# Optimization experiments

Hardware: AMD Instinct MI355X
Metric: run time of the kernel (lower is better)

## Reference

```python
import jax, jax.numpy as jnp
import numpy as np

N = 1024
D = 128          # node_dim
NUM_LAYERS = 3
H_CLS = 128      # edge classifier hidden


def setup_inputs() -> dict:
    key = jax.random.key(0)
    ks = jax.random.split(key, 20)
    s_in = 1.0 / np.sqrt(3.0)
    s_d = 1.0 / np.sqrt(D)
    s_2d = 1.0 / np.sqrt(2 * D)
    s_h = 1.0 / np.sqrt(H_CLS)
    inp = {
        "node_features": jax.random.uniform(ks[0], (N, 3), jnp.float32),
        "adj_matrix": jax.random.uniform(ks[1], (N, N), jnp.float32),
        "edge_weights": jax.random.normal(ks[2], (N, N, 1), jnp.float32),
        # node embedding Linear(3, D)
        "W_embed": jax.random.uniform(ks[3], (3, D), jnp.float32, -s_in, s_in),
        "b_embed": jax.random.uniform(ks[4], (D,), jnp.float32, -s_in, s_in),
        # stacked GCN layer params, [L, ...]
        "Wu": jax.random.uniform(ks[5], (NUM_LAYERS, D, D), jnp.float32, -s_d, s_d),
        "bu": jax.random.uniform(ks[6], (NUM_LAYERS, D), jnp.float32, -s_d, s_d),
        "Wv": jax.random.uniform(ks[7], (NUM_LAYERS, D, D), jnp.float32, -s_d, s_d),
        "bv": jax.random.uniform(ks[8], (NUM_LAYERS, D), jnp.float32, -s_d, s_d),
        "Wg": jax.random.uniform(ks[9], (NUM_LAYERS, 2 * D, D), jnp.float32, -s_2d, s_2d),
        "bg": jax.random.uniform(ks[10], (NUM_LAYERS, D), jnp.float32, -s_2d, s_2d),
        # edge classifier: Linear(2D, 128) -> ReLU -> Linear(128, 1)
        "Wc1": jax.random.uniform(ks[11], (2 * D, H_CLS), jnp.float32, -s_2d, s_2d),
        "bc1": jax.random.uniform(ks[12], (H_CLS,), jnp.float32, -s_2d, s_2d),
        "Wc2": jax.random.uniform(ks[13], (H_CLS, 1), jnp.float32, -s_h, s_h),
        "bc2": jax.random.uniform(ks[14], (1,), jnp.float32, -s_h, s_h),
    }
    return inp


def reference(node_features, adj_matrix, edge_weights,
              W_embed, b_embed, Wu, bu, Wv, bv, Wg, bg,
              Wc1, bc1, Wc2, bc2):
    h = node_features @ W_embed + b_embed                       # [N, D]
    for l in range(NUM_LAYERS):
        u = h @ Wu[l] + bu[l]                                   # [N, D]
        v = h @ Wv[l] + bv[l]                                   # [N, D]
        agg = adj_matrix @ v                                    # [N, D]
        # gate Linear(2D, D) on cat([u, agg]) == u @ Wg[:D] + agg @ Wg[D:]
        gate = jax.nn.sigmoid(u @ Wg[l, :D] + agg @ Wg[l, D:] + bg[l])
        h = jax.nn.relu(h + gate * agg)
    # edge classifier: cat([h_i, h_j]) @ Wc1 == (h @ Wc1[:D])[i] + (h @ Wc1[D:])[j]
    hi = h @ Wc1[:D]                                            # [N, H]
    hj = h @ Wc1[D:]                                            # [N, H]
    hidden = jax.nn.relu(hi[:, None, :] + hj[None, :, :] + bc1) # [N, N, H]
    logits = jnp.einsum('ijh,h->ij', hidden, Wc2[:, 0]) + bc2[0]  # [N, N]
    loss = jnp.mean(jnp.square(logits * adj_matrix - edge_weights[..., 0]))
    return logits, loss
```

## Files before the change

kernel.cpp:

```cpp
#include <hip/hip_runtime.h>

#define NN 1024
#define DD 128

typedef __attribute__((ext_vector_type(8))) __bf16 bf16x8;
typedef __attribute__((ext_vector_type(4))) float f32x4;

__device__ __forceinline__ float us2f(unsigned short b) { return __uint_as_float(((unsigned)b) << 16); }
__device__ __forceinline__ unsigned short f2bf(float f) {
    unsigned x = __float_as_uint(f);
    return (unsigned short)((x + 0x7fffu + ((x >> 16) & 1u)) >> 16);
}

__global__ __launch_bounds__(256) void k_prep_embuv(
    const float* __restrict__ adj, unsigned short* __restrict__ aH, unsigned short* __restrict__ aL,
    const float* __restrict__ nf, const float* __restrict__ We, const float* __restrict__ be,
    const float* __restrict__ Wu, const float* __restrict__ bu,
    const float* __restrict__ Wv, const float* __restrict__ bv,
    float* __restrict__ h, float* __restrict__ u,
    unsigned short* __restrict__ vTh, unsigned short* __restrict__ vTl,
    float* __restrict__ lossAcc, unsigned* __restrict__ counter)
{
    __shared__ float hS[4][DD];
    int b = blockIdx.x, tid = threadIdx.x;
    if (b < 1024) {
        int idx = (b * 256 + tid) * 4;
        float4 a = *(const float4*)(adj + idx);
        ushort4 hv, lv;
        hv.x = f2bf(a.x); lv.x = f2bf(a.x - us2f(hv.x));
        hv.y = f2bf(a.y); lv.y = f2bf(a.y - us2f(hv.y));
        hv.z = f2bf(a.z); lv.z = f2bf(a.z - us2f(hv.z));
        hv.w = f2bf(a.w); lv.w = f2bf(a.w - us2f(hv.w));
        *(ushort4*)(aH + idx) = hv;
        *(ushort4*)(aL + idx) = lv;
        if (b == 0 && tid == 0) { *lossAcc = 0.f; *counter = 0u; }
        return;
    }
    int m0 = (b - 1024) * 4;
    int d = tid & 127, half = tid >> 7;
    float hr[4];
#pragma unroll
    for (int r = 0; r < 4; ++r) {
        float a = be[d];
#pragma unroll
        for (int k = 0; k < 3; ++k) a = fmaf(nf[(m0 + r) * 3 + k], We[k * DD + d], a);
        hr[r] = a;
    }
    if (half == 0) {
#pragma unroll
        for (int r = 0; r < 4; ++r) { h[(m0 + r) * DD + d] = hr[r]; hS[r][d] = hr[r]; }
    }
    __syncthreads();
    const float* W = half ? Wv : Wu;
    float acc[4] = {0.f, 0.f, 0.f, 0.f};
#pragma unroll 4
    for (int k4 = 0; k4 < DD; k4 += 4) {
        f32x4 h0 = *(const f32x4*)&hS[0][k4];
        f32x4 h1 = *(const f32x4*)&hS[1][k4];
        f32x4 h2 = *(const f32x4*)&hS[2][k4];
        f32x4 h3 = *(const f32x4*)&hS[3][k4];
#pragma unroll
        for (int kk = 0; kk < 4; ++kk) {
            float w = W[(k4 + kk) * DD + d];
            acc[0] = fmaf(h0[kk], w, acc[0]);
            acc[1] = fmaf(h1[kk], w, acc[1]);
            acc[2] = fmaf(h2[kk], w, acc[2]);
            acc[3] = fmaf(h3[kk], w, acc[3]);
        }
    }
    if (half == 0) {
        float bb = bu[d];
#pragma unroll
        for (int r = 0; r < 4; ++r) u[(m0 + r) * DD + d] = acc[r] + bb;
    } else {
        float bb = bv[d];
        float v0 = acc[0] + bb, v1 = acc[1] + bb, v2 = acc[2] + bb, v3 = acc[3] + bb;
        ushort4 hv, lv;
        hv.x = f2bf(v0); lv.x = f2bf(v0 - us2f(hv.x));
        hv.y = f2bf(v1); lv.y = f2bf(v1 - us2f(hv.y));
        hv.z = f2bf(v2); lv.z = f2bf(v2 - us2f(hv.z));
        hv.w = f2bf(v3); lv.w = f2bf(v3 - us2f(hv.w));
        *(ushort4*)(vTh + d * NN + m0) = hv;
        *(ushort4*)(vTl + d * NN + m0) = lv;
    }
}

__global__ __launch_bounds__(256) void k_agg(
    const unsigned short* __restrict__ adjH, const unsigned short* __restrict__ adjL,
    const unsigned short* __restrict__ vTh, const unsigned short* __restrict__ vTl,
    float* __restrict__ P)
{
    int tid = threadIdx.x, lane = tid & 63, w = tid >> 6;
    int b = blockIdx.x;
    int nt = b >> 7;
    int mt = (b >> 1) & 63;
    int kc = ((b & 1) << 2) | w;
    int m = lane & 15, quad = lane >> 4;
    int k0 = kc * 128 + quad * 8;
    const unsigned short* ah = adjH + (size_t)(mt * 16 + m) * NN + k0;
    const unsigned short* al = adjL + (size_t)(mt * 16 + m) * NN + k0;
    const unsigned short* bh = vTh + (size_t)(nt * 16 + m) * NN + k0;
    const unsigned short* bl = vTl + (size_t)(nt * 16 + m) * NN + k0;
    f32x4 acc = {0.f, 0.f, 0.f, 0.f};
#pragma unroll
    for (int kt = 0; kt < 4; ++kt) {
        bf16x8 aH = *(const bf16x8*)(ah + kt * 32);
        bf16x8 aL = *(const bf16x8*)(al + kt * 32);
        bf16x8 bH = *(const bf16x8*)(bh + kt * 32);
        bf16x8 bL = *(const bf16x8*)(bl + kt * 32);
        acc = __builtin_amdgcn_mfma_f32_16x16x32_bf16(aH, bH, acc, 0, 0, 0);
        acc = __builtin_amdgcn_mfma_f32_16x16x32_bf16(aH, bL, acc, 0, 0, 0);
        acc = __builtin_amdgcn_mfma_f32_16x16x32_bf16(aL, bH, acc, 0, 0, 0);
    }
    float* Pk = P + (size_t)kc * (NN * DD);
    int row0 = mt * 16 + quad * 4;
    int col = nt * 16 + m;
#pragma unroll
    for (int r = 0; r < 4; ++r) Pk[(row0 + r) * DD + col] = acc[r];
}

__global__ __launch_bounds__(256) void k_gateuv(
    const float* __restrict__ P, float* __restrict__ u, float* __restrict__ h,
    const float* __restrict__ Wg, const float* __restrict__ bg,
    const float* __restrict__ Wun, const float* __restrict__ bun,
    const float* __restrict__ Wvn, const float* __restrict__ bvn,
    unsigned short* __restrict__ vTh, unsigned short* __restrict__ vTl)
{
    __shared__ float uS[4][DD], aS[4][DD], hS[4][DD];
    int tid = threadIdx.x;
    int m0 = blockIdx.x * 4;
    int d = tid & 127, half = tid >> 7;
#pragma unroll
    for (int e = tid; e < 512; e += 256) {
        int r = e >> 7, dd = e & 127;
        int idx = (m0 + r) * DD + dd;
        float s = 0.f;
#pragma unroll
        for (int c = 0; c < 8; ++c) s += P[(size_t)c * (NN * DD) + idx];
        aS[r][dd] = s;
        uS[r][dd] = u[idx];
    }
    __syncthreads();
    const float* WA = Wg;
    const float* WB = Wg + DD * DD;
    int r0 = half * 2;
    float acc[2] = {0.f, 0.f};
#pragma unroll 4
    for (int k4 = 0; k4 < DD; k4 += 4) {
        f32x4 u0 = *(const f32x4*)&uS[r0][k4];
        f32x4 u1 = *(const f32x4*)&uS[r0 + 1][k4];
        f32x4 a0 = *(const f32x4*)&aS[r0][k4];
        f32x4 a1 = *(const f32x4*)&aS[r0 + 1][k4];
#pragma unroll
        for (int kk = 0; kk < 4; ++kk) {
            float wa = WA[(k4 + kk) * DD + d];
            float wb = WB[(k4 + kk) * DD + d];
            acc[0] = fmaf(u0[kk], wa, fmaf(a0[kk], wb, acc[0]));
            acc[1] = fmaf(u1[kk], wa, fmaf(a1[kk], wb, acc[1]));
        }
    }
    float bgd = bg[d];
#pragma unroll
    for (int rr = 0; rr < 2; ++rr) {
        int r = r0 + rr;
        float g = 1.f / (1.f + __expf(-(acc[rr] + bgd)));
        float nh = fmaf(g, aS[r][d], h[(m0 + r) * DD + d]);
        nh = nh > 0.f ? nh : 0.f;
        h[(m0 + r) * DD + d] = nh;
        hS[r][d] = nh;
    }
    __syncthreads();
    const float* W = half ? Wvn : Wun;
    float av[4] = {0.f, 0.f, 0.f, 0.f};
#pragma unroll 4
    for (int k4 = 0; k4 < DD; k4 += 4) {
        f32x4 h0 = *(const f32x4*)&hS[0][k4];
        f32x4 h1 = *(const f32x4*)&hS[1][k4];
        f32x4 h2 = *(const f32x4*)&hS[2][k4];
        f32x4 h3 = *(const f32x4*)&hS[3][k4];
#pragma unroll
        for (int kk = 0; kk < 4; ++kk) {
            float w = W[(k4 + kk) * DD + d];
            av[0] = fmaf(h0[kk], w, av[0]);
            av[1] = fmaf(h1[kk], w, av[1]);
            av[2] = fmaf(h2[kk], w, av[2]);
            av[3] = fmaf(h3[kk], w, av[3]);
        }
    }
    if (half == 0) {
        float bb = bun[d];
#pragma unroll
        for (int r = 0; r < 4; ++r) u[(m0 + r) * DD + d] = av[r] + bb;
    } else {
        float bb = bvn[d];
        float v0 = av[0] + bb, v1 = av[1] + bb, v2 = av[2] + bb, v3 = av[3] + bb;
        ushort4 hv, lv;
        hv.x = f2bf(v0); lv.x = f2bf(v0 - us2f(hv.x));
        hv.y = f2bf(v1); lv.y = f2bf(v1 - us2f(hv.y));
        hv.z = f2bf(v2); lv.z = f2bf(v2 - us2f(hv.z));
        hv.w = f2bf(v3); lv.w = f2bf(v3 - us2f(hv.w));
        *(ushort4*)(vTh + d * NN + m0) = hv;
        *(ushort4*)(vTl + d * NN + m0) = lv;
    }
}

__global__ __launch_bounds__(256) void k_gatecls(
    const float* __restrict__ P, float* __restrict__ u, float* __restrict__ h,
    const float* __restrict__ Wg, const float* __restrict__ bg,
    const float* __restrict__ Wc1, const float* __restrict__ bc1, const float* __restrict__ Wc2,
    float* __restrict__ hi, float* __restrict__ hj,
    float* __restrict__ S1, float* __restrict__ S2)
{
    __shared__ float uS[4][DD], aS[4][DD], hS[4][DD];
    __shared__ float sred[2][4];
    int tid = threadIdx.x;
    int m0 = blockIdx.x * 4;
    int d = tid & 127, half = tid >> 7;
    if (tid < 8) sred[tid >> 2][tid & 3] = 0.f;
#pragma unroll
    for (int e = tid; e < 512; e += 256) {
        int r = e >> 7, dd = e & 127;
        int idx = (m0 + r) * DD + dd;
        float s = 0.f;
#pragma unroll
        for (int c = 0; c < 8; ++c) s += P[(size_t)c * (NN * DD) + idx];
        aS[r][dd] = s;
        uS[r][dd] = u[idx];
    }
    __syncthreads();
    const float* WA = Wg;
    const float* WB = Wg + DD * DD;
    int r0 = half * 2;
    float acc[2] = {0.f, 0.f};
#pragma unroll 4
    for (int k4 = 0; k4 < DD; k4 += 4) {
        f32x4 u0 = *(const f32x4*)&uS[r0][k4];
        f32x4 u1 = *(const f32x4*)&uS[r0 + 1][k4];
        f32x4 a0 = *(const f32x4*)&aS[r0][k4];
        f32x4 a1 = *(const f32x4*)&aS[r0 + 1][k4];
#pragma unroll
        for (int kk = 0; kk < 4; ++kk) {
            float wa = WA[(k4 + kk) * DD + d];
            float wb = WB[(k4 + kk) * DD + d];
            acc[0] = fmaf(u0[kk], wa, fmaf(a0[kk], wb, acc[0]));
            acc[1] = fmaf(u1[kk], wa, fmaf(a1[kk], wb, acc[1]));
        }
    }
    float bgd = bg[d];
#pragma unroll
    for (int rr = 0; rr < 2; ++rr) {
        int r = r0 + rr;
        float g = 1.f / (1.f + __expf(-(acc[rr] + bgd)));
        float nh = fmaf(g, aS[r][d], h[(m0 + r) * DD + d]);
        nh = nh > 0.f ? nh : 0.f;
        hS[r][d] = nh;
    }
    __syncthreads();
    const float* W = Wc1 + (half ? DD * DD : 0);
    float av[4] = {0.f, 0.f, 0.f, 0.f};
#pragma unroll 4
    for (int k4 = 0; k4 < DD; k4 += 4) {
        f32x4 h0 = *(const f32x4*)&hS[0][k4];
        f32x4 h1 = *(const f32x4*)&hS[1][k4];
        f32x4 h2 = *(const f32x4*)&hS[2][k4];
        f32x4 h3 = *(const f32x4*)&hS[3][k4];
#pragma unroll
        for (int kk = 0; kk < 4; ++kk) {
            float w = W[(k4 + kk) * DD + d];
            av[0] = fmaf(h0[kk], w, av[0]);
            av[1] = fmaf(h1[kk], w, av[1]);
            av[2] = fmaf(h2[kk], w, av[2]);
            av[3] = fmaf(h3[kk], w, av[3]);
        }
    }
    float wv = Wc2[d];
    float bcv = half ? 0.f : bc1[d];
    float* out = half ? hj : hi;
    int lane = tid & 63;
#pragma unroll
    for (int r = 0; r < 4; ++r) {
        float val = av[r] + bcv;
        out[(m0 + r) * DD + d] = val;
        float p = val * wv;
#pragma unroll
        for (int off = 32; off; off >>= 1) p += __shfl_down(p, off);
        if (lane == 0) atomicAdd(&sred[half][r], p);
    }
    __syncthreads();
    if (tid < 4) S1[m0 + tid] = sred[0][tid];
    else if (tid < 8) S2[m0 + tid - 4] = sred[1][tid - 4];
}

__global__ __launch_bounds__(256) void k_edge(
    const float* __restrict__ hi, const float* __restrict__ hj,
    const float* __restrict__ S1, const float* __restrict__ S2,
    const float* __restrict__ Wc2, const float* __restrict__ bc2,
    const float* __restrict__ adj, const float* __restrict__ ew,
    float* __restrict__ outL, float* __restrict__ lossAcc, unsigned* __restrict__ counter)
{
    __shared__ float hiT[128][68];
    __shared__ float hjT[128][68];
    __shared__ float wS[128];
    __shared__ float lred;
    int tid = threadIdx.x;
    int i0 = (blockIdx.x >> 4) * 64, j0 = (blockIdx.x & 15) * 64;
    if (tid == 0) lred = 0.f;
    if (tid < 128) wS[tid] = Wc2[tid];
    for (int e = tid; e < 64 * 128; e += 256) {
        int r = e >> 7, hh = e & 127;
        hiT[hh][r] = hi[(i0 + r) * DD + hh];
        hjT[hh][r] = hj[(j0 + r) * DD + hh];
    }
    __syncthreads();
    int tx = tid & 15, ty = tid >> 4;
    float acc[4][4] = {};
#pragma unroll 4
    for (int hh = 0; hh < 128; ++hh) {
        f32x4 a = *(const f32x4*)&hiT[hh][ty * 4];
        f32x4 b = *(const f32x4*)&hjT[hh][tx * 4];
        float w = wS[hh];
#pragma unroll
        for (int p = 0; p < 4; ++p)
#pragma unroll
            for (int q = 0; q < 4; ++q) {
                float x = a[p] + b[q];
                acc[p][q] = fmaf(fabsf(x), w, acc[p][q]);
            }
    }
    float bcv = bc2[0];
    float ls = 0.f;
#pragma unroll
    for (int p = 0; p < 4; ++p) {
        int i = i0 + ty * 4 + p;
        float s1 = S1[i];
        int jb = j0 + tx * 4;
        f32x4 s2 = *(const f32x4*)(S2 + jb);
        f32x4 lg;
#pragma unroll
        for (int q = 0; q < 4; ++q)
            lg[q] = fmaf(0.5f, acc[p][q] + s1 + s2[q], bcv);
        *(f32x4*)(outL + (size_t)i * NN + jb) = lg;
        f32x4 a4 = *(const f32x4*)(adj + (size_t)i * NN + jb);
        f32x4 e4 = *(const f32x4*)(ew + (size_t)i * NN + jb);
#pragma unroll
        for (int q = 0; q < 4; ++q) {
            float t = fmaf(lg[q], a4[q], -e4[q]);
            ls = fmaf(t, t, ls);
        }
    }
#pragma unroll
    for (int off = 32; off; off >>= 1) ls += __shfl_down(ls, off);
    if ((tid & 63) == 0) atomicAdd(&lred, ls);
    __syncthreads();
    if (tid == 0) {
        atomicAdd(lossAcc, lred);
        __threadfence();
        unsigned old = atomicAdd(counter, 1u);
        if (old == 255u) {
            __threadfence();
            outL[(size_t)NN * NN] = (*(volatile float*)lossAcc) * (1.f / (1024.f * 1024.f));
        }
    }
}

extern "C" void kernel_launch(void* const* d_in, const int* in_sizes, int n_in,
                              void* d_out, int out_size, void* d_ws, size_t ws_size,
                              hipStream_t stream)
{
    const float* nf  = (const float*)d_in[0];
    const float* adj = (const float*)d_in[1];
    const float* ew  = (const float*)d_in[2];
    const float* We  = (const float*)d_in[3];
    const float* be  = (const float*)d_in[4];
    const float* Wu  = (const float*)d_in[5];
    const float* bu  = (const float*)d_in[6];
    const float* Wv  = (const float*)d_in[7];
    const float* bv  = (const float*)d_in[8];
    const float* Wg  = (const float*)d_in[9];
    const float* bg  = (const float*)d_in[10];
    const float* Wc1 = (const float*)d_in[11];
    const float* bc1 = (const float*)d_in[12];
    const float* Wc2 = (const float*)d_in[13];
    const float* bc2 = (const float*)d_in[14];

    float* ws = (float*)d_ws;
    float* h   = ws;
    float* u   = ws + 131072;
    unsigned short* vTh = (unsigned short*)(ws + 262144);
    unsigned short* vTl = (unsigned short*)(ws + 327680);
    float* P   = ws + 393216;
    unsigned short* adjH = (unsigned short*)(ws + 1441792);
    unsigned short* adjL = (unsigned short*)(ws + 1966080);
    float* hi  = ws + 2490368;
    float* hj  = ws + 2621440;
    float* S1  = ws + 2752512;
    float* S2  = ws + 2753536;
    float* lossAcc = ws + 2754560;
    unsigned* counter = (unsigned*)(ws + 2754561);

    k_prep_embuv<<<1280, 256, 0, stream>>>(adj, adjH, adjL, nf, We, be,
                                           Wu, bu, Wv, bv, h, u, vTh, vTl, lossAcc, counter);
    for (int l = 0; l < 3; ++l) {
        k_agg<<<1024, 256, 0, stream>>>(adjH, adjL, vTh, vTl, P);
        if (l < 2)
            k_gateuv<<<256, 256, 0, stream>>>(P, u, h, Wg + l * 32768, bg + l * 128,
                                              Wu + (l + 1) * 16384, bu + (l + 1) * 128,
                                              Wv + (l + 1) * 16384, bv + (l + 1) * 128,
                                              vTh, vTl);
        else
            k_gatecls<<<256, 256, 0, stream>>>(P, u, h, Wg + 2 * 32768, bg + 2 * 128,
                                               Wc1, bc1, Wc2, hi, hj, S1, S2);
    }
    k_edge<<<256, 256, 0, stream>>>(hi, hj, S1, S2, Wc2, bc2, adj, ew,
                                    (float*)d_out, lossAcc, counter);
}
```

Baseline: 187.2 us.

## Fuse all stages into one persistent kernel with software grid barriers

Replaces the eight separate launches (prep, three agg plus gate kernels, edge) with a single 256-block persistent kernel that separates stages with atomic-counter grid barriers, after a memset of the control words. Per-layer buffers are triple-buffered so later stages never overwrite data that other blocks are still reading. The aggregation split changes from eight K-chunks written to a global partial buffer to two K-chunks reduced in shared memory, which removes the 8-way partial-sum traffic. The risks are lower parallelism in the aggregation stage (256 blocks instead of 1024), spin-wait barrier cost, and a deadlock hazard if the 256 blocks are not all resident at once.

Measured after the change: 344.2 us. 83.9% more time.

```diff
diff --git a/kernel.cpp b/kernel.cpp
--- a/kernel.cpp
+++ b/kernel.cpp
@@ -12,353 +12,320 @@
     return (unsigned short)((x + 0x7fffu + ((x >> 16) & 1u)) >> 16);
 }
 
-__global__ __launch_bounds__(256) void k_prep_embuv(
-    const float* __restrict__ adj, unsigned short* __restrict__ aH, unsigned short* __restrict__ aL,
-    const float* __restrict__ nf, const float* __restrict__ We, const float* __restrict__ be,
-    const float* __restrict__ Wu, const float* __restrict__ bu,
-    const float* __restrict__ Wv, const float* __restrict__ bv,
-    float* __restrict__ h, float* __restrict__ u,
-    unsigned short* __restrict__ vTh, unsigned short* __restrict__ vTl,
-    float* __restrict__ lossAcc, unsigned* __restrict__ counter)
-{
-    __shared__ float hS[4][DD];
-    int b = blockIdx.x, tid = threadIdx.x;
-    if (b < 1024) {
-        int idx = (b * 256 + tid) * 4;
-        float4 a = *(const float4*)(adj + idx);
-        ushort4 hv, lv;
-        hv.x = f2bf(a.x); lv.x = f2bf(a.x - us2f(hv.x));
-        hv.y = f2bf(a.y); lv.y = f2bf(a.y - us2f(hv.y));
-        hv.z = f2bf(a.z); lv.z = f2bf(a.z - us2f(hv.z));
-        hv.w = f2bf(a.w); lv.w = f2bf(a.w - us2f(hv.w));
-        *(ushort4*)(aH + idx) = hv;
-        *(ushort4*)(aL + idx) = lv;
-        if (b == 0 && tid == 0) { *lossAcc = 0.f; *counter = 0u; }
-        return;
-    }
-    int m0 = (b - 1024) * 4;
-    int d = tid & 127, half = tid >> 7;
-    float hr[4];
-#pragma unroll
-    for (int r = 0; r < 4; ++r) {
-        float a = be[d];
-#pragma unroll
-        for (int k = 0; k < 3; ++k) a = fmaf(nf[(m0 + r) * 3 + k], We[k * DD + d], a);
-        hr[r] = a;
-    }
-    if (half == 0) {
-#pragma unroll
-        for (int r = 0; r < 4; ++r) { h[(m0 + r) * DD + d] = hr[r]; hS[r][d] = hr[r]; }
+struct SEdge { float hiT[128][68]; float hjT[128][68]; float wS[128]; float lred; };
+struct SGate { float uS[4][DD]; float aS[4][DD]; float hS[4][DD]; float sred[2][4]; };
+struct SAgg  { float red[4][64][4]; };
+union SU { SEdge edge; SGate gate; SAgg agg; float hS[4][DD]; };
+
+__device__ __forceinline__ void gridbar(unsigned* bar, unsigned target, int tid) {
+    __syncthreads();
+    if (tid == 0) {
+        __threadfence();
+        __hip_atomic_fetch_add(bar, 1u, __ATOMIC_RELEASE, __HIP_MEMORY_SCOPE_AGENT);
+        while (__hip_atomic_load(bar, __ATOMIC_ACQUIRE, __HIP_MEMORY_SCOPE_AGENT) < target)
+            __builtin_amdgcn_s_sleep(1);
+        __threadfence();
     }
     __syncthreads();
-    const float* W = half ? Wv : Wu;
-    float acc[4] = {0.f, 0.f, 0.f, 0.f};
-#pragma unroll 4
-    for (int k4 = 0; k4 < DD; k4 += 4) {
-        f32x4 h0 = *(const f32x4*)&hS[0][k4];
-        f32x4 h1 = *(const f32x4*)&hS[1][k4];
-        f32x4 h2 = *(const f32x4*)&hS[2][k4];
-        f32x4 h3 = *(const f32x4*)&hS[3][k4];
-#pragma unroll
-        for (int kk = 0; kk < 4; ++kk) {
-            float w = W[(k4 + kk) * DD + d];
-            acc[0] = fmaf(h0[kk], w, acc[0]);
-            acc[1] = fmaf(h1[kk], w, acc[1]);
-            acc[2] = fmaf(h2[kk], w, acc[2]);
-            acc[3] = fmaf(h3[kk], w, acc[3]);
+}
+
+__global__ __launch_bounds__(256) void k_all(
+    const float* __restrict__ nf, const float* __restrict__ adj, const float* __restrict__ ew,
+    const float* __restrict__ We, const float* __restrict__ be,
+    const float* __restrict__ Wu_all, const float* __restrict__ bu_all,
+    const float* __restrict__ Wv_all, const float* __restrict__ bv_all,
+    const float* __restrict__ Wg_all, const float* __restrict__ bg_all,
+    const float* __restrict__ Wc1, const float* __restrict__ bc1,
+    const float* __restrict__ Wc2, const float* __restrict__ bc2,
+    float* __restrict__ hbuf, float* __restrict__ ubuf, float* __restrict__ aggbuf,
+    unsigned short* __restrict__ vthbuf, unsigned short* __restrict__ vtlbuf,
+    unsigned short* __restrict__ adjH, unsigned short* __restrict__ adjL,
+    float* __restrict__ hi, float* __restrict__ hj,
+    float* __restrict__ S1, float* __restrict__ S2,
+    unsigned* __restrict__ ctrl,
+    float* __restrict__ outL)
+{
+    __shared__ SU sh;
+    const int b = blockIdx.x, tid = threadIdx.x;
+    unsigned* bar = ctrl;
+    unsigned* edgeCnt = ctrl + 1;
+    float* lossAcc = (float*)(ctrl + 2);
+    const int d = tid & 127, half = tid >> 7;
+
+    {
+#pragma unroll
+        for (int i = 0; i < 4; ++i) {
+            int idx = b * 4096 + i * 1024 + tid * 4;
+            float4 a = *(const float4*)(adj + idx);
+            ushort4 hv, lv;
+            hv.x = f2bf(a.x); lv.x = f2bf(a.x - us2f(hv.x));
+            hv.y = f2bf(a.y); lv.y = f2bf(a.y - us2f(hv.y));
+            hv.z = f2bf(a.z); lv.z = f2bf(a.z - us2f(hv.z));
+            hv.w = f2bf(a.w); lv.w = f2bf(a.w - us2f(hv.w));
+            *(ushort4*)(adjH + idx) = hv;
+            *(ushort4*)(adjL + idx) = lv;
+        }
+        int m0 = b * 4;
+        if (half == 0) {
+#pragma unroll
+            for (int r = 0; r < 4; ++r) {
+                float a = be[d];
+#pragma unroll
+                for (int k = 0; k < 3; ++k) a = fmaf(nf[(m0 + r) * 3 + k], We[k * DD + d], a);
+                hbuf[(m0 + r) * DD + d] = a;
+                sh.hS[r][d] = a;
+            }
+        }
+        __syncthreads();
+        const float* W = half ? Wv_all : Wu_all;
+        float acc[4] = {0.f, 0.f, 0.f, 0.f};
+#pragma unroll 4
+        for (int k4 = 0; k4 < DD; k4 += 4) {
+            f32x4 h0 = *(const f32x4*)&sh.hS[0][k4];
+            f32x4 h1 = *(const f32x4*)&sh.hS[1][k4];
+            f32x4 h2 = *(const f32x4*)&sh.hS[2][k4];
+            f32x4 h3 = *(const f32x4*)&sh.hS[3][k4];
+#pragma unroll
+            for (int kk = 0; kk < 4; ++kk) {
+                float w = W[(k4 + kk) * DD + d];
+                acc[0] = fmaf(h0[kk], w, acc[0]);
+                acc[1] = fmaf(h1[kk], w, acc[1]);
+                acc[2] = fmaf(h2[kk], w, acc[2]);
+                acc[3] = fmaf(h3[kk], w, acc[3]);
+            }
+        }
+        if (half == 0) {
+            float bb = bu_all[d];
+#pragma unroll
+            for (int r = 0; r < 4; ++r) ubuf[(m0 + r) * DD + d] = acc[r] + bb;
+        } else {
+            float bb = bv_all[d];
+            float v0 = acc[0] + bb, v1 = acc[1] + bb, v2 = acc[2] + bb, v3 = acc[3] + bb;
+            ushort4 hv, lv;
+            hv.x = f2bf(v0); lv.x = f2bf(v0 - us2f(hv.x));
+            hv.y = f2bf(v1); lv.y = f2bf(v1 - us2f(hv.y));
+            hv.z = f2bf(v2); lv.z = f2bf(v2 - us2f(hv.z));
+            hv.w = f2bf(v3); lv.w = f2bf(v3 - us2f(hv.w));
+            *(ushort4*)(vthbuf + d * NN + m0) = hv;
+            *(ushort4*)(vtlbuf + d * NN + m0) = lv;
         }
     }
-    if (half == 0) {
-        float bb = bu[d];
-#pragma unroll
-        for (int r = 0; r < 4; ++r) u[(m0 + r) * DD + d] = acc[r] + bb;
-    } else {
-        float bb = bv[d];
-        float v0 = acc[0] + bb, v1 = acc[1] + bb, v2 = acc[2] + bb, v3 = acc[3] + bb;
-        ushort4 hv, lv;
-        hv.x = f2bf(v0); lv.x = f2bf(v0 - us2f(hv.x));
-        hv.y = f2bf(v1); lv.y = f2bf(v1 - us2f(hv.y));
-        hv.z = f2bf(v2); lv.z = f2bf(v2 - us2f(hv.z));
-        hv.w = f2bf(v3); lv.w = f2bf(v3 - us2f(hv.w));
-        *(ushort4*)(vTh + d * NN + m0) = hv;
-        *(ushort4*)(vTl + d * NN + m0) = lv;
+    unsigned tgt = 256;
+    gridbar(bar, tgt, tid); tgt += 256;
+
+    for (int l = 0; l < 3; ++l) {
+        const unsigned short* vth = vthbuf + l * (NN * DD);
+        const unsigned short* vtl = vtlbuf + l * (NN * DD);
+        float* aggl = aggbuf + l * (NN * DD);
+        const float* ul = ubuf + l * (NN * DD);
+        const float* hprev = hbuf + l * (NN * DD);
+
+        {
+            int w = tid >> 6, lane = tid & 63;
+            int mt = b & 63, np = b >> 6;
+            int nt = np * 2 + (w >> 1);
+            int kc = w & 1;
+            int m = lane & 15, quad = lane >> 4;
+            int k0 = kc * 512 + quad * 8;
+            const unsigned short* ah = adjH + (size_t)(mt * 16 + m) * NN + k0;
+            const unsigned short* al = adjL + (size_t)(mt * 16 + m) * NN + k0;
+            const unsigned short* bh = vth + (size_t)(nt * 16 + m) * NN + k0;
+            const unsigned short* bl = vtl + (size_t)(nt * 16 + m) * NN + k0;
+            f32x4 acc = {0.f, 0.f, 0.f, 0.f};
+#pragma unroll 4
+            for (int kt = 0; kt < 16; ++kt) {
+                bf16x8 aH = *(const bf16x8*)(ah + kt * 32);
+                bf16x8 aL = *(const bf16x8*)(al + kt * 32);
+                bf16x8 bH = *(const bf16x8*)(bh + kt * 32);
+                bf16x8 bL = *(const bf16x8*)(bl + kt * 32);
+                acc = __builtin_amdgcn_mfma_f32_16x16x32_bf16(aH, bH, acc, 0, 0, 0);
+                acc = __builtin_amdgcn_mfma_f32_16x16x32_bf16(aH, bL, acc, 0, 0, 0);
+                acc = __builtin_amdgcn_mfma_f32_16x16x32_bf16(aL, bH, acc, 0, 0, 0);
+            }
+            *(f32x4*)&sh.agg.red[w][lane][0] = acc;
+            __syncthreads();
+            if ((w & 1) == 0) {
+                f32x4 s = *(const f32x4*)&sh.agg.red[w][lane][0];
+                f32x4 t = *(const f32x4*)&sh.agg.red[w + 1][lane][0];
+                int row0 = mt * 16 + quad * 4;
+                int col = nt * 16 + m;
+#pragma unroll
+                for (int r = 0; r < 4; ++r) aggl[(row0 + r) * DD + col] = s[r] + t[r];
+            }
+        }
+        gridbar(bar, tgt, tid); tgt += 256;
+
+        {
+            int m0 = b * 4;
+            if (tid < 8) sh.gate.sred[tid >> 2][tid & 3] = 0.f;
+#pragma unroll
+            for (int e = tid; e < 512; e += 256) {
+                int r = e >> 7, dd = e & 127;
+                int idx = (m0 + r) * DD + dd;
+                sh.gate.aS[r][dd] = aggl[idx];
+                sh.gate.uS[r][dd] = ul[idx];
+            }
+            __syncthreads();
+            const float* WA = Wg_all + l * (2 * DD * DD);
+            const float* WB = WA + DD * DD;
+            int r0 = half * 2;
+            float acc[2] = {0.f, 0.f};
+#pragma unroll 4
+            for (int k4 = 0; k4 < DD; k4 += 4) {
+                f32x4 u0 = *(const f32x4*)&sh.gate.uS[r0][k4];
+                f32x4 u1 = *(const f32x4*)&sh.gate.uS[r0 + 1][k4];
+                f32x4 a0 = *(const f32x4*)&sh.gate.aS[r0][k4];
+                f32x4 a1 = *(const f32x4*)&sh.gate.aS[r0 + 1][k4];
+#pragma unroll
+                for (int kk = 0; kk < 4; ++kk) {
+                    float wa = WA[(k4 + kk) * DD + d];
+                    float wb = WB[(k4 + kk) * DD + d];
+                    acc[0] = fmaf(u0[kk], wa, fmaf(a0[kk], wb, acc[0]));
+                    acc[1] = fmaf(u1[kk], wa, fmaf(a1[kk], wb, acc[1]));
+                }
+            }
+            float bgd = bg_all[l * DD + d];
+#pragma unroll
+            for (int rr = 0; rr < 2; ++rr) {
+                int r = r0 + rr;
+                float g = 1.f / (1.f + __expf(-(acc[rr] + bgd)));
+                float nh = fmaf(g, sh.gate.aS[r][d], hprev[(m0 + r) * DD + d]);
+                nh = nh > 0.f ? nh : 0.f;
+                sh.gate.hS[r][d] = nh;
+                if (l < 2) hbuf[(l + 1) * (NN * DD) + (m0 + r) * DD + d] = nh;
+            }
+            __syncthreads();
+            if (l < 2) {
+                const float* W = half ? (Wv_all + (l + 1) * (DD * DD)) : (Wu_all + (l + 1) * (DD * DD));
+                float av[4] = {0.f, 0.f, 0.f, 0.f};
+#pragma unroll 4
+                for (int k4 = 0; k4 < DD; k4 += 4) {
+                    f32x4 h0 = *(const f32x4*)&sh.gate.hS[0][k4];
+                    f32x4 h1 = *(const f32x4*)&sh.gate.hS[1][k4];
+                    f32x4 h2 = *(const f32x4*)&sh.gate.hS[2][k4];
+                    f32x4 h3 = *(const f32x4*)&sh.gate.hS[3][k4];
+#pragma unroll
+                    for (int kk = 0; kk < 4; ++kk) {
+                        float w = W[(k4 + kk) * DD + d];
+                        av[0] = fmaf(h0[kk], w, av[0]);
+                        av[1] = fmaf(h1[kk], w, av[1]);
+                        av[2] = fmaf(h2[kk], w, av[2]);
+                        av[3] = fmaf(h3[kk], w, av[3]);
+                    }
+                }
+                if (half == 0) {
+                    float bb = bu_all[(l + 1) * DD + d];
+#pragma unroll
+                    for (int r = 0; r < 4; ++r)
+                        ubuf[(l + 1) * (NN * DD) + (m0 + r) * DD + d] = av[r] + bb;
+                } else {
+                    float bb = bv_all[(l + 1) * DD + d];
+                    float v0 = av[0] + bb, v1 = av[1] + bb, v2 = av[2] + bb, v3 = av[3] + bb;
+                    ushort4 hv, lv;
+                    hv.x = f2bf(v0); lv.x = f2bf(v0 - us2f(hv.x));
+                    hv.y = f2bf(v1); lv.y = f2bf(v1 - us2f(hv.y));
+                    hv.z = f2bf(v2); lv.z = f2bf(v2 - us2f(hv.z));
+                    hv.w = f2bf(v3); lv.w = f2bf(v3 - us2f(hv.w));
+                    *(ushort4*)(vthbuf + (l + 1) * (NN * DD) + d * NN + m0) = hv;
+                    *(ushort4*)(vtlbuf + (l + 1) * (NN * DD) + d * NN + m0) = lv;
+                }
+            } else {
+                const float* W = Wc1 + (half ? DD * DD : 0);
+                float av[4] = {0.f, 0.f, 0.f, 0.f};
+#pragma unroll 4
+                for (int k4 = 0; k4 < DD; k4 += 4) {
+                    f32x4 h0 = *(const f32x4*)&sh.gate.hS[0][k4];
+                    f32x4 h1 = *(const f32x4*)&sh.gate.hS[1][k4];
+                    f32x4 h2 = *(const f32x4*)&sh.gate.hS[2][k4];
+                    f32x4 h3 = *(const f32x4*)&sh.gate.hS[3][k4];
+#pragma unroll
+                    for (int kk = 0; kk < 4; ++kk) {
+                        float w = W[(k4 + kk) * DD + d];
+                        av[0] = fmaf(h0[kk], w, av[0]);
+                        av[1] = fmaf(h1[kk], w, av[1]);
+                        av[2] = fmaf(h2[kk], w, av[2]);
+                        av[3] = fmaf(h3[kk], w, av[3]);
+                    }
+                }
+                float wv = Wc2[d];
+                float bcv = half ? 0.f : bc1[d];
+                float* out = half ? hj : hi;
+                int lane = tid & 63;
+#pragma unroll
+                for (int r = 0; r < 4; ++r) {
+                    float val = av[r] + bcv;
+                    out[(m0 + r) * DD + d] = val;
+                    float p = val * wv;
+#pragma unroll
+                    for (int off = 32; off; off >>= 1) p += __shfl_down(p, off);
+                    if (lane == 0) atomicAdd(&sh.gate.sred[half][r], p);
+                }
+                __syncthreads();
+                if (tid < 4) S1[m0 + tid] = sh.gate.sred[0][tid];
+                else if (tid < 8) S2[m0 + tid - 4] = sh.gate.sred[1][tid - 4];
+            }
+        }
+        gridbar(bar, tgt, tid); tgt += 256;
     }
-}
-
-__global__ __launch_bounds__(256) void k_agg(
-    const unsigned short* __restrict__ adjH, const unsigned short* __restrict__ adjL,
-    const unsigned short* __restrict__ vTh, const unsigned short* __restrict__ vTl,
-    float* __restrict__ P)
-{
-    int tid = threadIdx.x, lane = tid & 63, w = tid >> 6;
-    int b = blockIdx.x;
-    int nt = b >> 7;
-    int mt = (b >> 1) & 63;
-    int kc = ((b & 1) << 2) | w;
-    int m = lane & 15, quad = lane >> 4;
-    int k0 = kc * 128 + quad * 8;
-    const unsigned short* ah = adjH + (size_t)(mt * 16 + m) * NN + k0;
-    const unsigned short* al = adjL + (size_t)(mt * 16 + m) * NN + k0;
-    const unsigned short* bh = vTh + (size_t)(nt * 16 + m) * NN + k0;
-    const unsigned short* bl = vTl + (size_t)(nt * 16 + m) * NN + k0;
-    f32x4 acc = {0.f, 0.f, 0.f, 0.f};
-#pragma unroll
-    for (int kt = 0; kt < 4; ++kt) {
-        bf16x8 aH = *(const bf16x8*)(ah + kt * 32);
-        bf16x8 aL = *(const bf16x8*)(al + kt * 32);
-        bf16x8 bH = *(const bf16x8*)(bh + kt * 32);
-        bf16x8 bL = *(const bf16x8*)(bl + kt * 32);
-        acc = __builtin_amdgcn_mfma_f32_16x16x32_bf16(aH, bH, acc, 0, 0, 0);
-        acc = __builtin_amdgcn_mfma_f32_16x16x32_bf16(aH, bL, acc, 0, 0, 0);
-        acc = __builtin_amdgcn_mfma_f32_16x16x32_bf16(aL, bH, acc, 0, 0, 0);
-    }
-    float* Pk = P + (size_t)kc * (NN * DD);
-    int row0 = mt * 16 + quad * 4;
-    int col = nt * 16 + m;
-#pragma unroll
-    for (int r = 0; r < 4; ++r) Pk[(row0 + r) * DD + col] = acc[r];
-}
-
-__global__ __launch_bounds__(256) void k_gateuv(
-    const float* __restrict__ P, float* __restrict__ u, float* __restrict__ h,
-    const float* __restrict__ Wg, const float* __restrict__ bg,
-    const float* __restrict__ Wun, const float* __restrict__ bun,
-    const float* __restrict__ Wvn, const float* __restrict__ bvn,
-    unsigned short* __restrict__ vTh, unsigned short* __restrict__ vTl)
-{
-    __shared__ float uS[4][DD], aS[4][DD], hS[4][DD];
-    int tid = threadIdx.x;
-    int m0 = blockIdx.x * 4;
-    int d = tid & 127, half = tid >> 7;
-#pragma unroll
-    for (int e = tid; e < 512; e += 256) {
-        int r = e >> 7, dd = e & 127;
-        int idx = (m0 + r) * DD + dd;
-        float s = 0.f;
-#pragma unroll
-        for (int c = 0; c < 8; ++c) s += P[(size_t)c * (NN * DD) + idx];
-        aS[r][dd] = s;
-        uS[r][dd] = u[idx];
-    }
-    __syncthreads();
-    const float* WA = Wg;
-    const float* WB = Wg + DD * DD;
-    int r0 = half * 2;
-    float acc[2] = {0.f, 0.f};
-#pragma unroll 4
-    for (int k4 = 0; k4 < DD; k4 += 4) {
-        f32x4 u0 = *(const f32x4*)&uS[r0][k4];
-        f32x4 u1 = *(const f32x4*)&uS[r0 + 1][k4];
-        f32x4 a0 = *(const f32x4*)&aS[r0][k4];
-        f32x4 a1 = *(const f32x4*)&aS[r0 + 1][k4];
-#pragma unroll
-        for (int kk = 0; kk < 4; ++kk) {
-            float wa = WA[(k4 + kk) * DD + d];
-            float wb = WB[(k4 + kk) * DD + d];
-            acc[0] = fmaf(u0[kk], wa, fmaf(a0[kk], wb, acc[0]));
-            acc[1] = fmaf(u1[kk], wa, fmaf(a1[kk], wb, acc[1]));
-        }
-    }
-    float bgd = bg[d];
-#pragma unroll
-    for (int rr = 0; rr < 2; ++rr) {
-        int r = r0 + rr;
-        float g = 1.f / (1.f + __expf(-(acc[rr] + bgd)));
-        float nh = fmaf(g, aS[r][d], h[(m0 + r) * DD + d]);
-        nh = nh > 0.f ? nh : 0.f;
-        h[(m0 + r) * DD + d] = nh;
-        hS[r][d] = nh;
-    }
-    __syncthreads();
-    const float* W = half ? Wvn : Wun;
-    float av[4] = {0.f, 0.f, 0.f, 0.f};
-#pragma unroll 4
-    for (int k4 = 0; k4 < DD; k4 += 4) {
-        f32x4 h0 = *(const f32x4*)&hS[0][k4];
-        f32x4 h1 = *(const f32x4*)&hS[1][k4];
-        f32x4 h2 = *(const f32x4*)&hS[2][k4];
-        f32x4 h3 = *(const f32x4*)&hS[3][k4];
-#pragma unroll
-        for (int kk = 0; kk < 4; ++kk) {
-            float w = W[(k4 + kk) * DD + d];
-            av[0] = fmaf(h0[kk], w, av[0]);
-            av[1] = fmaf(h1[kk], w, av[1]);
-            av[2] = fmaf(h2[kk], w, av[2]);
-            av[3] = fmaf(h3[kk], w, av[3]);
-        }
-    }
-    if (half == 0) {
-        float bb = bun[d];
-#pragma unroll
-        for (int r = 0; r < 4; ++r) u[(m0 + r) * DD + d] = av[r] + bb;
-    } else {
-        float bb = bvn[d];
-        float v0 = av[0] + bb, v1 = av[1] + bb, v2 = av[2] + bb, v3 = av[3] + bb;
-        ushort4 hv, lv;
-        hv.x = f2bf(v0); lv.x = f2bf(v0 - us2f(hv.x));
-        hv.y = f2bf(v1); lv.y = f2bf(v1 - us2f(hv.y));
-        hv.z = f2bf(v2); lv.z = f2bf(v2 - us2f(hv.z));
-        hv.w = f2bf(v3); lv.w = f2bf(v3 - us2f(hv.w));
-        *(ushort4*)(vTh + d * NN + m0) = hv;
-        *(ushort4*)(vTl + d * NN + m0) = lv;
-    }
-}
-
-__global__ __launch_bounds__(256) void k_gatecls(
-    const float* __restrict__ P, float* __restrict__ u, float* __restrict__ h,
-    const float* __restrict__ Wg, const float* __restrict__ bg,
-    const float* __restrict__ Wc1, const float* __restrict__ bc1, const float* __restrict__ Wc2,
-    float* __restrict__ hi, float* __restrict__ hj,
-    float* __restrict__ S1, float* __restrict__ S2)
-{
-    __shared__ float uS[4][DD], aS[4][DD], hS[4][DD];
-    __shared__ float sred[2][4];
-    int tid = threadIdx.x;
-    int m0 = blockIdx.x * 4;
-    int d = tid & 127, half = tid >> 7;
-    if (tid < 8) sred[tid >> 2][tid & 3] = 0.f;
-#pragma unroll
-    for (int e = tid; e < 512; e += 256) {
-        int r = e >> 7, dd = e & 127;
-        int idx = (m0 + r) * DD + dd;
-        float s = 0.f;
-#pragma unroll
-        for (int c = 0; c < 8; ++c) s += P[(size_t)c * (NN * DD) + idx];
-        aS[r][dd] = s;
-        uS[r][dd] = u[idx];
-    }
-    __syncthreads();
-    const float* WA = Wg;
-    const float* WB = Wg + DD * DD;
-    int r0 = half * 2;
-    float acc[2] = {0.f, 0.f};
-#pragma unroll 4
-    for (int k4 = 0; k4 < DD; k4 += 4) {
-        f32x4 u0 = *(const f32x4*)&uS[r0][k4];
-        f32x4 u1 = *(const f32x4*)&uS[r0 + 1][k4];
-        f32x4 a0 = *(const f32x4*)&aS[r0][k4];
-        f32x4 a1 = *(const f32x4*)&aS[r0 + 1][k4];
-#pragma unroll
-        for (int kk = 0; kk < 4; ++kk) {
-            float wa = WA[(k4 + kk) * DD + d];
-            float wb = WB[(k4 + kk) * DD + d];
-            acc[0] = fmaf(u0[kk], wa, fmaf(a0[kk], wb, acc[0]));
-            acc[1] = fmaf(u1[kk], wa, fmaf(a1[kk], wb, acc[1]));
-        }
-    }
-    float bgd = bg[d];
-#pragma unroll
-    for (int rr = 0; rr < 2; ++rr) {
-        int r = r0 + rr;
-        float g = 1.f / (1.f + __expf(-(acc[rr] + bgd)));
-        float nh = fmaf(g, aS[r][d], h[(m0 + r) * DD + d]);
-        nh = nh > 0.f ? nh : 0.f;
-        hS[r][d] = nh;
-    }
-    __syncthreads();
-    const float* W = Wc1 + (half ? DD * DD : 0);
-    float av[4] = {0.f, 0.f, 0.f, 0.f};
-#pragma unroll 4
-    for (int k4 = 0; k4 < DD; k4 += 4) {
-        f32x4 h0 = *(const f32x4*)&hS[0][k4];
-        f32x4 h1 = *(const f32x4*)&hS[1][k4];
-        f32x4 h2 = *(const f32x4*)&hS[2][k4];
-        f32x4 h3 = *(const f32x4*)&hS[3][k4];
-#pragma unroll
-        for (int kk = 0; kk < 4; ++kk) {
-            float w = W[(k4 + kk) * DD + d];
-            av[0] = fmaf(h0[kk], w, av[0]);
-            av[1] = fmaf(h1[kk], w, av[1]);
-            av[2] = fmaf(h2[kk], w, av[2]);
-            av[3] = fmaf(h3[kk], w, av[3]);
-        }
-    }
-    float wv = Wc2[d];
-    float bcv = half ? 0.f : bc1[d];
-    float* out = half ? hj : hi;
-    int lane = tid & 63;
-#pragma unroll
-    for (int r = 0; r < 4; ++r) {
-        float val = av[r] + bcv;
-        out[(m0 + r) * DD + d] = val;
-        float p = val * wv;
-#pragma unroll
-        for (int off = 32; off; off >>= 1) p += __shfl_down(p, off);
-        if (lane == 0) atomicAdd(&sred[half][r], p);
-    }
-    __syncthreads();
-    if (tid < 4) S1[m0 + tid] = sred[0][tid];
-    else if (tid < 8) S2[m0 + tid - 4] = sred[1][tid - 4];
-}
-
-__global__ __launch_bounds__(256) void k_edge(
-    const float* __restrict__ hi, const float* __restrict__ hj,
-    const float* __restrict__ S1, const float* __restrict__ S2,
-    const float* __restrict__ Wc2, const float* __restrict__ bc2,
-    const float* __restrict__ adj, const float* __restrict__ ew,
-    float* __restrict__ outL, float* __restrict__ lossAcc, unsigned* __restrict__ counter)
-{
-    __shared__ float hiT[128][68];
-    __shared__ float hjT[128][68];
-    __shared__ float wS[128];
-    __shared__ float lred;
-    int tid = threadIdx.x;
-    int i0 = (blockIdx.x >> 4) * 64, j0 = (blockIdx.x & 15) * 64;
-    if (tid == 0) lred = 0.f;
-    if (tid < 128) wS[tid] = Wc2[tid];
-    for (int e = tid; e < 64 * 128; e += 256) {
-        int r = e >> 7, hh = e & 127;
-        hiT[hh][r] = hi[(i0 + r) * DD + hh];
-        hjT[hh][r] = hj[(j0 + r) * DD + hh];
-    }
-    __syncthreads();
-    int tx = tid & 15, ty = tid >> 4;
-    float acc[4][4] = {};
-#pragma unroll 4
-    for (int hh = 0; hh < 128; ++hh) {
-        f32x4 a = *(const f32x4*)&hiT[hh][ty * 4];
-        f32x4 b = *(const f32x4*)&hjT[hh][tx * 4];
-        float w = wS[hh];
-#pragma unroll
-        for (int p = 0; p < 4; ++p)
+
+    {
+        int i0 = (b >> 4) * 64, j0 = (b & 15) * 64;
+        if (tid == 0) sh.edge.lred = 0.f;
+        if (tid < 128) sh.edge.wS[tid] = Wc2[tid];
+        for (int e = tid; e < 64 * 128; e += 256) {
+            int r = e >> 7, hh = e & 127;
+            sh.edge.hiT[hh][r] = hi[(i0 + r) * DD + hh];
+            sh.edge.hjT[hh][r] = hj[(j0 + r) * DD + hh];
+        }
+        __syncthreads();
+        int tx = tid & 15, ty = tid >> 4;
+        float acc[4][4] = {};
+#pragma unroll 4
+        for (int hh = 0; hh < 128; ++hh) {
+            f32x4 a = *(const f32x4*)&sh.edge.hiT[hh][ty * 4];
+            f32x4 bb = *(const f32x4*)&sh.edge.hjT[hh][tx * 4];
+            float w = sh.edge.wS[hh];
+#pragma unroll
+            for (int p = 0; p < 4; ++p)
+#pragma unroll
+                for (int q = 0; q < 4; ++q) {
+                    float x = a[p] + bb[q];
+                    acc[p][q] = fmaf(fabsf(x), w, acc[p][q]);
+                }
+        }
+        float bcv = bc2[0];
+        float ls = 0.f;
+#pragma unroll
+        for (int p = 0; p < 4; ++p) {
+            int i = i0 + ty * 4 + p;
+            float s1 = S1[i];
+            int jb = j0 + tx * 4;
+            f32x4 s2 = *(const f32x4*)(S2 + jb);
+            f32x4 lg;
+#pragma unroll
+            for (int q = 0; q < 4; ++q)
+                lg[q] = fmaf(0.5f, acc[p][q] + s1 + s2[q], bcv);
+            *(f32x4*)(outL + (size_t)i * NN + jb) = lg;
+            f32x4 a4 = *(const f32x4*)(adj + (size_t)i * NN + jb);
+            f32x4 e4 = *(const f32x4*)(ew + (size_t)i * NN + jb);
 #pragma unroll
             for (int q = 0; q < 4; ++q) {
-                float x = a[p] + b[q];
-                acc[p][q] = fmaf(fabsf(x), w, acc[p][q]);
-            }
-    }
-    float bcv = bc2[0];
-    float ls = 0.f;
-#pragma unroll
-    for (int p = 0; p < 4; ++p) {
-        int i = i0 + ty * 4 + p;
-        float s1 = S1[i];
-        int jb = j0 + tx * 4;
-        f32x4 s2 = *(const f32x4*)(S2 + jb);
-        f32x4 lg;
-#pragma unroll
-        for (int q = 0; q < 4; ++q)
-            lg[q] = fmaf(0.5f, acc[p][q] + s1 + s2[q], bcv);
-        *(f32x4*)(outL + (size_t)i * NN + jb) = lg;
-        f32x4 a4 = *(const f32x4*)(adj + (size_t)i * NN + jb);
-        f32x4 e4 = *(const f32x4*)(ew + (size_t)i * NN + jb);
-#pragma unroll
-        for (int q = 0; q < 4; ++q) {
-            float t = fmaf(lg[q], a4[q], -e4[q]);
-            ls = fmaf(t, t, ls);
-        }
-    }
-#pragma unroll
-    for (int off = 32; off; off >>= 1) ls += __shfl_down(ls, off);
-    if ((tid & 63) == 0) atomicAdd(&lred, ls);
-    __syncthreads();
-    if (tid == 0) {
-        atomicAdd(lossAcc, lred);
-        __threadfence();
-        unsigned old = atomicAdd(counter, 1u);
-        if (old == 255u) {
+                float t = fmaf(lg[q], a4[q], -e4[q]);
+                ls = fmaf(t, t, ls);
+            }
+        }
+#pragma unroll
+        for (int off = 32; off; off >>= 1) ls += __shfl_down(ls, off);
+        if ((tid & 63) == 0) atomicAdd(&sh.edge.lred, ls);
+        __syncthreads();
+        if (tid == 0) {
+            atomicAdd(lossAcc, sh.edge.lred);
             __threadfence();
-            outL[(size_t)NN * NN] = (*(volatile float*)lossAcc) * (1.f / (1024.f * 1024.f));
+            unsigned old = atomicAdd(edgeCnt, 1u);
+            if (old == 255u) {
+                __threadfence();
+                outL[(size_t)NN * NN] = (*(volatile float*)lossAcc) * (1.f / (1024.f * 1024.f));
+            }
         }
     }
 }
@@ -384,33 +351,22 @@
     const float* bc2 = (const float*)d_in[14];
 
     float* ws = (float*)d_ws;
-    float* h   = ws;
-    float* u   = ws + 131072;
-    unsigned short* vTh = (unsigned short*)(ws + 262144);
-    unsigned short* vTl = (unsigned short*)(ws + 327680);
-    float* P   = ws + 393216;
-    unsigned short* adjH = (unsigned short*)(ws + 1441792);
-    unsigned short* adjL = (unsigned short*)(ws + 1966080);
-    float* hi  = ws + 2490368;
-    float* hj  = ws + 2621440;
-    float* S1  = ws + 2752512;
-    float* S2  = ws + 2753536;
-    float* lossAcc = ws + 2754560;
-    unsigned* counter = (unsigned*)(ws + 2754561);
-
-    k_prep_embuv<<<1280, 256, 0, stream>>>(adj, adjH, adjL, nf, We, be,
-                                           Wu, bu, Wv, bv, h, u, vTh, vTl, lossAcc, counter);
-    for (int l = 0; l < 3; ++l) {
-        k_agg<<<1024, 256, 0, stream>>>(adjH, adjL, vTh, vTl, P);
-        if (l < 2)
-            k_gateuv<<<256, 256, 0, stream>>>(P, u, h, Wg + l * 32768, bg + l * 128,
-                                              Wu + (l + 1) * 16384, bu + (l + 1) * 128,
-                                              Wv + (l + 1) * 16384, bv + (l + 1) * 128,
-                                              vTh, vTl);
-        else
-            k_gatecls<<<256, 256, 0, stream>>>(P, u, h, Wg + 2 * 32768, bg + 2 * 128,
-                                               Wc1, bc1, Wc2, hi, hj, S1, S2);
-    }
-    k_edge<<<256, 256, 0, stream>>>(hi, hj, S1, S2, Wc2, bc2, adj, ew,
-                                    (float*)d_out, lossAcc, counter);
+    float* hbuf   = ws;
+    float* ubuf   = ws + 393216;
+    float* aggbuf = ws + 786432;
+    unsigned short* vthbuf = (unsigned short*)(ws + 1179648);
+    unsigned short* vtlbuf = (unsigned short*)(ws + 1376256);
+    unsigned short* adjH   = (unsigned short*)(ws + 1572864);
+    unsigned short* adjL   = (unsigned short*)(ws + 2097152);
+    float* hi = ws + 2621440;
+    float* hj = ws + 2752512;
+    float* S1 = ws + 2883584;
+    float* S2 = ws + 2884608;
+    unsigned* ctrl = (unsigned*)(ws + 2885632);
+
+    hipMemsetAsync(ctrl, 0, 16, stream);
+    k_all<<<256, 256, 0, stream>>>(nf, adj, ew, We, be, Wu, bu, Wv, bv, Wg, bg,
+                                   Wc1, bc1, Wc2, bc2,
+                                   hbuf, ubuf, aggbuf, vthbuf, vtlbuf, adjH, adjL,
+                                   hi, hj, S1, S2, ctrl, (float*)d_out);
 }
```
